# Kernel optimization log

Hardware: AMD Instinct MI355X
Metric: run time of the kernel (lower is better)

## Reference

```python
import jax, jax.numpy as jnp
import numpy as np

N_NODES = 10000
N_EDGES = 320000
IN_DIM = 256
HID = 64
HEADS = 4
OUT_DIM = 64
NEG_SLOPE = 0.2


def setup_inputs() -> dict:
    key = jax.random.key(0)
    ks = jax.random.split(key, 10)
    s = 0.05
    return {
        "h": jax.random.normal(ks[0], (N_NODES, IN_DIM), jnp.float32),
        "src": jax.random.randint(ks[1], (N_EDGES,), 0, N_NODES, jnp.int32),
        "dst": jax.random.randint(ks[2], (N_EDGES,), 0, N_NODES, jnp.int32),
        "W1": jax.random.normal(ks[3], (IN_DIM, HEADS * HID), jnp.float32) * s,
        "al1": jax.random.normal(ks[4], (HEADS, HID), jnp.float32) * s,
        "ar1": jax.random.normal(ks[5], (HEADS, HID), jnp.float32) * s,
        "b1": jnp.zeros((HEADS * HID,), jnp.float32),
        "W2": jax.random.normal(ks[6], (HEADS * HID, OUT_DIM), jnp.float32) * s,
        "al2": jax.random.normal(ks[7], (1, OUT_DIM), jnp.float32) * s,
        "ar2": jax.random.normal(ks[8], (1, OUT_DIM), jnp.float32) * s,
        "b2": jnp.zeros((OUT_DIM,), jnp.float32),
    }


def _gatconv(h, W, al, ar, b, src, dst, n_heads, d_out):
    """DGL-style GATConv: project, edge-softmax attention, scatter-aggregate."""
    n = h.shape[0]
    feat = (h @ W).reshape(n, n_heads, d_out)          # [N,H,D]
    el = jnp.sum(feat * al, axis=-1)                   # [N,H]
    er = jnp.sum(feat * ar, axis=-1)                   # [N,H]
    e = jax.nn.leaky_relu(el[src] + er[dst], NEG_SLOPE)  # [E,H]
    # segment softmax over incoming edges of each dst node
    m = jax.ops.segment_max(e, dst, num_segments=n)    # [N,H]
    ex = jnp.exp(e - m[dst])                           # [E,H]
    denom = jax.ops.segment_sum(ex, dst, num_segments=n)  # [N,H]
    alpha = ex / denom[dst]                            # [E,H]
    msg = feat[src] * alpha[:, :, None]                # [E,H,D]
    out = jax.ops.segment_sum(msg, dst, num_segments=n)  # [N,H,D]
    return out + b.reshape(n_heads, d_out)


def reference(h, src, dst, W1, al1, ar1, b1, W2, al2, ar2, b2):
    h1 = _gatconv(h, W1, al1, ar1, b1, src, dst, HEADS, HID)
    h1 = jax.nn.elu(h1.reshape(N_NODES, HEADS * HID))  # flatten(1) then ELU
    h2 = _gatconv(h1, W2, al2, ar2, b2, src, dst, 1, OUT_DIM)
    return jnp.squeeze(h2, axis=1)  # [N, OUT_DIM]
```

## Files before the change

kernel.cpp:

```cpp
#include <hip/hip_runtime.h>
#include <hip/hip_bf16.h>
#include <stdint.h>

#define NN 10000
#define NE 320000
#define NH 4
#define BCAP 128

#define GEMM1_MB 79
#define GEMM1_BLOCKS (GEMM1_MB * 4)
#define BUILD_BLOCKS 1250

typedef __attribute__((ext_vector_type(8))) short s16x8;
typedef __attribute__((ext_vector_type(4))) float f32x4;
typedef __attribute__((ext_vector_type(8))) unsigned short u16x8;

static __device__ __forceinline__ float b2f(unsigned short u) {
    union { unsigned int i; float f; } x; x.i = ((unsigned int)u) << 16; return x.f;
}
static __device__ __forceinline__ unsigned short f2b(float f) {
    unsigned int u = __float_as_uint(f);
    unsigned int r = (u + 0x7fffu + ((u >> 16) & 1u)) >> 16;
    return (unsigned short)r;
}

__global__ __launch_bounds__(256) void k_prep(const unsigned short* __restrict__ hraw,
                        const void* __restrict__ W1, const void* __restrict__ W2,
                        const void* al1, const void* ar1, const void* b1,
                        const void* al2, const void* ar2, const void* b2,
                        unsigned short* __restrict__ W1T, unsigned short* __restrict__ W2T,
                        unsigned short* __restrict__ canon, int* __restrict__ cnt,
                        int* __restrict__ flag) {
    __shared__ int sb[256];
    int t = threadIdx.x;
    int c = 0;
    for (int i = t; i < 2048; i += 256) {
        unsigned short u = hraw[i];
        int e = (u >> 7) & 0xFF;
        c += (e >= 97 && e <= 157) ? 1 : 0;
    }
    sb[t] = c;
    __syncthreads();
    for (int o = 128; o > 0; o >>= 1) {
        if (t < o) sb[t] += sb[t + o];
        __syncthreads();
    }
    int isbf = (sb[0] >= 1741) ? 1 : 0;

    int idx = blockIdx.x * 256 + t;
    if (idx < 65536) {
        int n = idx >> 8, k = idx & 255;
        W1T[idx] = isbf ? ((const unsigned short*)W1)[k * 256 + n]
                        : f2b(((const float*)W1)[k * 256 + n]);
    } else if (idx < 81920) {
        int j = idx - 65536;
        int n = j >> 8, k = j & 255;
        W2T[j] = isbf ? ((const unsigned short*)W2)[k * 64 + n]
                      : f2b(((const float*)W2)[k * 64 + n]);
    } else if (idx < 82880) {
        int j = idx - 81920;
        const void* srcp; int q;
        if      (j < 256) { srcp = al1; q = j; }
        else if (j < 512) { srcp = ar1; q = j - 256; }
        else if (j < 768) { srcp = b1;  q = j - 512; }
        else if (j < 832) { srcp = al2; q = j - 768; }
        else if (j < 896) { srcp = ar2; q = j - 832; }
        else              { srcp = b2;  q = j - 896; }
        canon[j] = isbf ? ((const unsigned short*)srcp)[q] : f2b(((const float*)srcp)[q]);
    } else if (idx < 92880) {
        cnt[idx - 82880] = 0;
    } else if (idx == 92880) {
        flag[0] = isbf;
    }
}

#define BSTRIDE 264
static __device__ __forceinline__ void gemm_body(short* Bs,
                        const void* __restrict__ A, const unsigned short* __restrict__ BT,
                        unsigned short* __restrict__ C,
                        float* __restrict__ el, float* __restrict__ er,
                        const unsigned short* __restrict__ al,
                        const unsigned short* __restrict__ ar,
                        int M, int N, int H, int a_isbf, int mtile, int head) {
    int t = threadIdx.x;
    int wave = t >> 6, lane = t & 63;
    int m0 = mtile * 128;
    const unsigned short* Bh = BT + (size_t)head * 64 * 256;

#pragma unroll
    for (int i = 0; i < 8; ++i) {
        int idx = t + i * 256;
        int row = idx >> 5, chunk = idx & 31;
        *(s16x8*)&Bs[row * BSTRIDE + chunk * 8] =
            *(const s16x8*)&Bh[(size_t)row * 256 + chunk * 8];
    }
    __syncthreads();

    int kq = (lane >> 4) * 8;
    const unsigned short* Ab = (const unsigned short*)A;
    const float*          Af = (const float*)A;
    int aR[2];
#pragma unroll
    for (int mi = 0; mi < 2; ++mi) {
        int aRow = m0 + mi * 64 + wave * 16 + (lane & 15);
        aR[mi] = (aRow < M) ? aRow : M - 1;
    }
    f32x4 acc[2][4] = {};

#pragma unroll
    for (int k0 = 0; k0 < 256; k0 += 32) {
        s16x8 afr[2];
#pragma unroll
        for (int mi = 0; mi < 2; ++mi) {
            if (a_isbf) {
                afr[mi] = *(const s16x8*)&Ab[(size_t)aR[mi] * 256 + k0 + kq];
            } else {
                const float* pf = &Af[(size_t)aR[mi] * 256 + k0 + kq];
                float4 x0 = *(const float4*)pf;
                float4 x1 = *(const float4*)(pf + 4);
                afr[mi][0] = (short)f2b(x0.x); afr[mi][1] = (short)f2b(x0.y);
                afr[mi][2] = (short)f2b(x0.z); afr[mi][3] = (short)f2b(x0.w);
                afr[mi][4] = (short)f2b(x1.x); afr[mi][5] = (short)f2b(x1.y);
                afr[mi][6] = (short)f2b(x1.z); afr[mi][7] = (short)f2b(x1.w);
            }
        }
#pragma unroll
        for (int nt = 0; nt < 4; ++nt) {
            s16x8 bfr = *(const s16x8*)&Bs[(nt * 16 + (lane & 15)) * BSTRIDE + k0 + kq];
            acc[0][nt] = __builtin_amdgcn_mfma_f32_16x16x32_bf16(afr[0], bfr, acc[0][nt], 0, 0, 0);
            acc[1][nt] = __builtin_amdgcn_mfma_f32_16x16x32_bf16(afr[1], bfr, acc[1][nt], 0, 0, 0);
        }
    }

    float alv[4], arv[4];
#pragma unroll
    for (int nt = 0; nt < 4; ++nt) {
        int c = (lane & 15) + nt * 16;
        alv[nt] = b2f(al[head * 64 + c]);
        arv[nt] = b2f(ar[head * 64 + c]);
    }
    int col0 = head * 64 + (lane & 15);
#pragma unroll
    for (int mi = 0; mi < 2; ++mi) {
        int r0 = m0 + mi * 64 + wave * 16 + (lane >> 4) * 4;
        float cr[4][4];
#pragma unroll
        for (int nt = 0; nt < 4; ++nt) {
            int col = col0 + nt * 16;
#pragma unroll
            for (int i = 0; i < 4; ++i) {
                unsigned short cb = f2b(acc[mi][nt][i]);
                cr[nt][i] = b2f(cb);
                int r = r0 + i;
                if (r < M) C[(size_t)r * N + col] = cb;
            }
        }
#pragma unroll
        for (int i = 0; i < 4; ++i) {
            float pl = 0.f, pr = 0.f;
#pragma unroll
            for (int nt = 0; nt < 4; ++nt) {
                pl += cr[nt][i] * alv[nt];
                pr += cr[nt][i] * arv[nt];
            }
#pragma unroll
            for (int o = 1; o < 16; o <<= 1) {
                pl += __shfl_xor(pl, o, 64);
                pr += __shfl_xor(pr, o, 64);
            }
            int r = r0 + i;
            if ((lane & 15) == 0 && r < M) {
                el[(size_t)r * H + head] = pl;
                er[(size_t)r * H + head] = pr;
            }
        }
    }
}

__global__ __launch_bounds__(256) void k_g1b(const void* __restrict__ A,
                        const unsigned short* __restrict__ W1T,
                        unsigned short* __restrict__ feat1,
                        float* __restrict__ el, float* __restrict__ er,
                        const unsigned short* __restrict__ al,
                        const unsigned short* __restrict__ ar,
                        const int* __restrict__ flagp,
                        const int* __restrict__ src, const int* __restrict__ dst,
                        int* __restrict__ cnt, int* __restrict__ bucket) {
    __shared__ short Bs[64 * BSTRIDE];
    int bid = blockIdx.x;
    if (bid < GEMM1_BLOCKS) {
        int head = bid / GEMM1_MB;
        int mtile = bid - head * GEMM1_MB;
        gemm_body(Bs, A, W1T, feat1, el, er, al, ar, NN, 256, NH, flagp[0], mtile, head);
    } else {
        int i = (bid - GEMM1_BLOCKS) * 256 + threadIdx.x;
        if (i < NE) {
            int d = dst[i];
            int pos = atomicAdd(&cnt[d], 1);
            if (pos < BCAP) bucket[(d << 7) + pos] = src[i];
        }
    }
}

static __device__ __forceinline__ void edge1_unit(int node,
                        const int* __restrict__ cnt, const int* __restrict__ bucket,
                        const float* __restrict__ el, const float* __restrict__ er,
                        const unsigned short* __restrict__ feat,
                        const unsigned short* __restrict__ b1,
                        unsigned short* __restrict__ h1row, int lane) {
    int eg = lane >> 3, d8 = lane & 7;
    int end = cnt[node]; if (end > BCAP) end = BCAP;
    const int* bkt = bucket + ((size_t)node << 7);
    float4 er4 = *(const float4*)&er[(size_t)node * 4];

    if (end <= 64) {
        int s = 0;
        float w0 = 0.f, w1 = 0.f, w2 = 0.f, w3 = 0.f;
        if (lane < end) {
            s = bkt[lane];
            float4 el4 = *(const float4*)&el[(size_t)s * 4];
            float x0 = el4.x + er4.x; x0 = (x0 >= 0.f) ? x0 : 0.2f * x0;
            float x1 = el4.y + er4.y; x1 = (x1 >= 0.f) ? x1 : 0.2f * x1;
            float x2 = el4.z + er4.z; x2 = (x2 >= 0.f) ? x2 : 0.2f * x2;
            float x3 = el4.w + er4.w; x3 = (x3 >= 0.f) ? x3 : 0.2f * x3;
            w0 = __expf(x0); w1 = __expf(x1);
            w2 = __expf(x2); w3 = __expf(x3);
        }
        int niter = (end + 7) >> 3;
#pragma unroll
        for (int h = 0; h < 4; ++h) {
            float wh = (h == 0) ? w0 : (h == 1) ? w1 : (h == 2) ? w2 : w3;
            float a[8] = {};
            for (int i = 0; i < niter; ++i) {
                int idx = 8 * i + eg;
                float we = __shfl(wh, idx, 64);
                int   se = __shfl(s, idx, 64);
                u16x8 fv = *(const u16x8*)&feat[(((size_t)se * NH + h) << 6) + (d8 << 3)];
#pragma unroll
                for (int j = 0; j < 8; ++j) a[j] += we * b2f(fv[j]);
            }
            float ls = wh;
#pragma unroll
            for (int o = 1; o < 64; o <<= 1) ls += __shfl_xor(ls, o, 64);
#pragma unroll
            for (int j = 0; j < 8; ++j) {
                a[j] += __shfl_xor(a[j], 8, 64);
                a[j] += __shfl_xor(a[j], 16, 64);
                a[j] += __shfl_xor(a[j], 32, 64);
            }
            if (eg == 0) {
                float inv = (ls > 0.f) ? 1.f / ls : 0.f;
                u16x8 r;
#pragma unroll
                for (int j = 0; j < 8; ++j) {
                    float o = a[j] * inv + b2f(b1[h * 64 + d8 * 8 + j]);
                    o = (o > 0.f) ? o : (__expf(o) - 1.f);
                    r[j] = f2b(o);
                }
                *(u16x8*)&h1row[h * 64 + d8 * 8] = r;
            }
        }
    } else {
        float a[4][8] = {};
        float ls0 = 0.f, ls1 = 0.f, ls2 = 0.f, ls3 = 0.f;
        for (int base = 0; base < end; base += 64) {
            int c = base + lane;
            int s = 0;
            float w0 = 0.f, w1 = 0.f, w2 = 0.f, w3 = 0.f;
            if (c < end) {
                s = bkt[c];
                float4 el4 = *(const float4*)&el[(size_t)s * 4];
                float x0 = el4.x + er4.x; x0 = (x0 >= 0.f) ? x0 : 0.2f * x0;
                float x1 = el4.y + er4.y; x1 = (x1 >= 0.f) ? x1 : 0.2f * x1;
                float x2 = el4.z + er4.z; x2 = (x2 >= 0.f) ? x2 : 0.2f * x2;
                float x3 = el4.w + er4.w; x3 = (x3 >= 0.f) ? x3 : 0.2f * x3;
                w0 = __expf(x0); w1 = __expf(x1);
                w2 = __expf(x2); w3 = __expf(x3);
            }
            ls0 += w0; ls1 += w1; ls2 += w2; ls3 += w3;
            int cn = end - base; if (cn > 64) cn = 64;
            int niter = (cn + 7) >> 3;
#pragma unroll
            for (int h = 0; h < 4; ++h) {
                float wh = (h == 0) ? w0 : (h == 1) ? w1 : (h == 2) ? w2 : w3;
                for (int i = 0; i < niter; ++i) {
                    int idx = 8 * i + eg;
                    float we = __shfl(wh, idx, 64);
                    int   se = __shfl(s, idx, 64);
                    u16x8 fv = *(const u16x8*)&feat[(((size_t)se * NH + h) << 6) + (d8 << 3)];
#pragma unroll
                    for (int j = 0; j < 8; ++j) a[h][j] += we * b2f(fv[j]);
                }
            }
        }
#pragma unroll
        for (int h = 0; h < 4; ++h) {
            float ls = (h == 0) ? ls0 : (h == 1) ? ls1 : (h == 2) ? ls2 : ls3;
#pragma unroll
            for (int o = 1; o < 64; o <<= 1) ls += __shfl_xor(ls, o, 64);
#pragma unroll
            for (int j = 0; j < 8; ++j) {
                a[h][j] += __shfl_xor(a[h][j], 8, 64);
                a[h][j] += __shfl_xor(a[h][j], 16, 64);
                a[h][j] += __shfl_xor(a[h][j], 32, 64);
            }
            if (eg == 0) {
                float inv = (ls > 0.f) ? 1.f / ls : 0.f;
                u16x8 r;
#pragma unroll
                for (int j = 0; j < 8; ++j) {
                    float o = a[h][j] * inv + b2f(b1[h * 64 + d8 * 8 + j]);
                    o = (o > 0.f) ? o : (__expf(o) - 1.f);
                    r[j] = f2b(o);
                }
                *(u16x8*)&h1row[h * 64 + d8 * 8] = r;
            }
        }
    }
}

#define H1S 264
__global__ __launch_bounds__(512, 4) void k_e1g2(const int* __restrict__ cnt,
                        const int* __restrict__ bucket,
                        const float* __restrict__ el, const float* __restrict__ er,
                        const unsigned short* __restrict__ feat,
                        const unsigned short* __restrict__ b1,
                        const unsigned short* __restrict__ W2T,
                        const unsigned short* __restrict__ al2,
                        const unsigned short* __restrict__ ar2,
                        unsigned short* __restrict__ feat2,
                        float* __restrict__ el2, float* __restrict__ er2) {
    __shared__ unsigned short h1s[16 * H1S];
    __shared__ unsigned short f2s[16 * 72];
    int t = threadIdx.x;
    int wave = t >> 6, lane = t & 63;
    int nb0 = blockIdx.x * 16;

#pragma unroll
    for (int r = 0; r < 2; ++r) {
        int lrow = wave * 2 + r;
        edge1_unit(nb0 + lrow, cnt, bucket, el, er, feat, b1, &h1s[lrow * H1S], lane);
    }
    __syncthreads();

    if (wave < 4) {
        int m = lane & 15;
        int kq = (lane >> 4) * 8;
        int colB = wave * 16 + m;
        const unsigned short* wp = &W2T[(size_t)colB * 256];
        f32x4 acc = {};
#pragma unroll
        for (int k0 = 0; k0 < 256; k0 += 32) {
            s16x8 af = *(const s16x8*)&h1s[m * H1S + k0 + kq];
            s16x8 bf = *(const s16x8*)&wp[k0 + kq];
            acc = __builtin_amdgcn_mfma_f32_16x16x32_bf16(af, bf, acc, 0, 0, 0);
        }
        int r0 = (lane >> 4) * 4;
#pragma unroll
        for (int i = 0; i < 4; ++i) {
            unsigned short cb = f2b(acc[i]);
            int row = r0 + i;
            feat2[(size_t)(nb0 + row) * 64 + colB] = cb;
            f2s[row * 72 + colB] = cb;
        }
    }
    __syncthreads();

    if (wave == 0) {
        int c = lane & 15;
        float alv[4], arv[4];
#pragma unroll
        for (int nt = 0; nt < 4; ++nt) {
            alv[nt] = b2f(al2[c + nt * 16]);
            arv[nt] = b2f(ar2[c + nt * 16]);
        }
        int r0 = (lane >> 4) * 4;
#pragma unroll
        for (int i = 0; i < 4; ++i) {
            int row = r0 + i;
            float cr[4];
#pragma unroll
            for (int nt = 0; nt < 4; ++nt) cr[nt] = b2f(f2s[row * 72 + c + nt * 16]);
            float pl = 0.f, pr = 0.f;
#pragma unroll
            for (int nt = 0; nt < 4; ++nt) {
                pl += cr[nt] * alv[nt];
                pr += cr[nt] * arv[nt];
            }
#pragma unroll
            for (int o = 1; o < 16; o <<= 1) {
                pl += __shfl_xor(pl, o, 64);
                pr += __shfl_xor(pr, o, 64);
            }
            if ((lane & 15) == 0) {
                el2[nb0 + row] = pl;
                er2[nb0 + row] = pr;
            }
        }
    }
}

__global__ __launch_bounds__(256) void k_edge2(const int* __restrict__ cnt,
                        const int* __restrict__ bucket,
                        const float* __restrict__ el, const float* __restrict__ er,
                        const unsigned short* __restrict__ feat,
                        const unsigned short* __restrict__ b2,
                        void* __restrict__ out, const int* __restrict__ flagp) {
    int wave = threadIdx.x >> 6, lane = threadIdx.x & 63;
    int node = blockIdx.x * 4 + wave;
    if (node >= NN) return;
    int eg = lane >> 3, d8 = lane & 7;
    int isbf = flagp[0];
    int end = cnt[node]; if (end > BCAP) end = BCAP;
    const int* bkt = bucket + ((size_t)node << 7);
    float er_d = er[node];
    float lsum = 0.f;
    float a[8] = {};
    for (int base = 0; base < end; base += 64) {
        int c = base + lane;
        float wgt = 0.f; int s = 0;
        if (c < end) {
            s = bkt[c];
            float x = el[s] + er_d;
            x = (x >= 0.f) ? x : 0.2f * x;
            wgt = __expf(x);
        }
        lsum += wgt;
        int cn = end - base; if (cn > 64) cn = 64;
        int niter = (cn + 7) >> 3;
#pragma unroll 2
        for (int i = 0; i < niter; ++i) {
            int idx = 8 * i + eg;
            float we = __shfl(wgt, idx, 64);
            int   se = __shfl(s, idx, 64);
            u16x8 fv = *(const u16x8*)&feat[((size_t)se << 6) + (d8 << 3)];
#pragma unroll
            for (int j = 0; j < 8; ++j) a[j] += we * b2f(fv[j]);
        }
    }
#pragma unroll
    for (int o = 1; o < 64; o <<= 1) lsum += __shfl_xor(lsum, o, 64);
#pragma unroll
    for (int j = 0; j < 8; ++j) {
        a[j] += __shfl_xor(a[j], 8, 64);
        a[j] += __shfl_xor(a[j], 16, 64);
        a[j] += __shfl_xor(a[j], 32, 64);
    }
    if (eg == 0) {
        float inv = (lsum > 0.f) ? 1.f / lsum : 0.f;
        float o[8];
#pragma unroll
        for (int j = 0; j < 8; ++j) o[j] = a[j] * inv + b2f(b2[d8 * 8 + j]);
        size_t ob = ((size_t)node << 6) + d8 * 8;
        if (isbf) {
            u16x8 r;
#pragma unroll
            for (int j = 0; j < 8; ++j) r[j] = f2b(o[j]);
            *(u16x8*)&((unsigned short*)out)[ob] = r;
        } else {
            float4 r0, r1;
            r0.x = o[0]; r0.y = o[1]; r0.z = o[2]; r0.w = o[3];
            r1.x = o[4]; r1.y = o[5]; r1.z = o[6]; r1.w = o[7];
            *(float4*)&((float*)out)[ob] = r0;
            *(float4*)&((float*)out)[ob + 4] = r1;
        }
    }
}

extern "C" void kernel_launch(void* const* d_in, const int* in_sizes, int n_in,
                              void* d_out, int out_size, void* d_ws, size_t ws_size,
                              hipStream_t stream) {
    const void* h   = d_in[0];
    const int*  src = (const int*)d_in[1];
    const int*  dst = (const int*)d_in[2];
    const void* W1  = d_in[3];
    const void* al1 = d_in[4];
    const void* ar1 = d_in[5];
    const void* b1  = d_in[6];
    const void* W2  = d_in[7];
    const void* al2 = d_in[8];
    const void* ar2 = d_in[9];
    const void* b2  = d_in[10];

    char* w = (char*)d_ws;
    size_t off = 0;
    auto alloc = [&](size_t bytes) -> void* {
        void* p = w + off;
        off = (off + bytes + 255) & ~(size_t)255;
        return p;
    };
    int* flag               = (int*)alloc(8);
    int* cnt                = (int*)alloc(NN * 4);
    int* bucket             = (int*)alloc((size_t)NN * BCAP * 4);
    unsigned short* canon   = (unsigned short*)alloc(960 * 2);
    unsigned short* W1T     = (unsigned short*)alloc(256 * 256 * 2);
    unsigned short* W2T     = (unsigned short*)alloc(64 * 256 * 2);
    unsigned short* feat1   = (unsigned short*)alloc((size_t)NN * 256 * 2);
    float* el1              = (float*)alloc(NN * NH * 4);
    float* er1              = (float*)alloc(NN * NH * 4);
    unsigned short* feat2   = (unsigned short*)alloc((size_t)NN * 64 * 2);
    float* el2              = (float*)alloc(NN * 4);
    float* er2              = (float*)alloc(NN * 4);
    (void)ws_size; (void)in_sizes; (void)n_in; (void)out_size;

    unsigned short* cal1 = canon + 0;
    unsigned short* car1 = canon + 256;
    unsigned short* cb1  = canon + 512;
    unsigned short* cal2 = canon + 768;
    unsigned short* car2 = canon + 832;
    unsigned short* cb2  = canon + 896;

    k_prep<<<363, 256, 0, stream>>>((const unsigned short*)h, W1, W2,
                                    al1, ar1, b1, al2, ar2, b2,
                                    W1T, W2T, canon, cnt, flag);
    k_g1b<<<GEMM1_BLOCKS + BUILD_BLOCKS, 256, 0, stream>>>(h, W1T, feat1, el1, er1,
                                                           cal1, car1, flag,
                                                           src, dst, cnt, bucket);
    k_e1g2<<<NN / 16, 512, 0, stream>>>(cnt, bucket, el1, er1, feat1, cb1,
                                        W2T, cal2, car2, feat2, el2, er2);
    k_edge2<<<(NN + 3) / 4, 256, 0, stream>>>(cnt, bucket, el2, er2, feat2, cb2, d_out, flag);
}
```

Measured before the change: 159.1 us.

## Fuse head loop in edge aggregation, halve e1g2 block size, fast-path edge2

In the layer-1 edge aggregation for nodes with at most 64 edges, the four per-head passes are merged into one loop. It loads all four head slices of each source row per iteration, shuffles the source index only once, and accumulates four accumulators at the same time. The fused edge+GEMM2 kernel now uses 256-thread blocks covering 8 nodes instead of 512 threads covering 16, so all four waves run the MFMA and rows past 8 are masked off. The layer-2 edge kernel gets a single-chunk fast path with deeper unrolling. These changes aim for more memory-level parallelism and better load balance, at the cost of higher register pressure from 32 accumulators and half-wasted MFMA rows.

```diff
diff --git a/kernel.cpp b/kernel.cpp
--- a/kernel.cpp
+++ b/kernel.cpp
@@ -226,34 +226,54 @@
             w0 = __expf(x0); w1 = __expf(x1);
             w2 = __expf(x2); w3 = __expf(x3);
         }
+        float ls0 = w0, ls1 = w1, ls2 = w2, ls3 = w3;
+#pragma unroll
+        for (int o = 1; o < 64; o <<= 1) {
+            ls0 += __shfl_xor(ls0, o, 64);
+            ls1 += __shfl_xor(ls1, o, 64);
+            ls2 += __shfl_xor(ls2, o, 64);
+            ls3 += __shfl_xor(ls3, o, 64);
+        }
+        float a0[8] = {}, a1[8] = {}, a2[8] = {}, a3[8] = {};
         int niter = (end + 7) >> 3;
-#pragma unroll
-        for (int h = 0; h < 4; ++h) {
-            float wh = (h == 0) ? w0 : (h == 1) ? w1 : (h == 2) ? w2 : w3;
-            float a[8] = {};
-            for (int i = 0; i < niter; ++i) {
-                int idx = 8 * i + eg;
-                float we = __shfl(wh, idx, 64);
-                int   se = __shfl(s, idx, 64);
-                u16x8 fv = *(const u16x8*)&feat[(((size_t)se * NH + h) << 6) + (d8 << 3)];
-#pragma unroll
-                for (int j = 0; j < 8; ++j) a[j] += we * b2f(fv[j]);
-            }
-            float ls = wh;
-#pragma unroll
-            for (int o = 1; o < 64; o <<= 1) ls += __shfl_xor(ls, o, 64);
+#pragma unroll 2
+        for (int i = 0; i < niter; ++i) {
+            int idx = 8 * i + eg;
+            int   se  = __shfl(s, idx, 64);
+            float we0 = __shfl(w0, idx, 64);
+            float we1 = __shfl(w1, idx, 64);
+            float we2 = __shfl(w2, idx, 64);
+            float we3 = __shfl(w3, idx, 64);
+            const u16x8* fp = (const u16x8*)(feat + ((size_t)se << 8));
+            u16x8 f0 = fp[d8];
+            u16x8 f1 = fp[8 + d8];
+            u16x8 f2 = fp[16 + d8];
+            u16x8 f3 = fp[24 + d8];
 #pragma unroll
             for (int j = 0; j < 8; ++j) {
-                a[j] += __shfl_xor(a[j], 8, 64);
-                a[j] += __shfl_xor(a[j], 16, 64);
-                a[j] += __shfl_xor(a[j], 32, 64);
-            }
-            if (eg == 0) {
+                a0[j] += we0 * b2f(f0[j]);
+                a1[j] += we1 * b2f(f1[j]);
+                a2[j] += we2 * b2f(f2[j]);
+                a3[j] += we3 * b2f(f3[j]);
+            }
+        }
+#pragma unroll
+        for (int j = 0; j < 8; ++j) {
+            a0[j] += __shfl_xor(a0[j], 8, 64);  a0[j] += __shfl_xor(a0[j], 16, 64);  a0[j] += __shfl_xor(a0[j], 32, 64);
+            a1[j] += __shfl_xor(a1[j], 8, 64);  a1[j] += __shfl_xor(a1[j], 16, 64);  a1[j] += __shfl_xor(a1[j], 32, 64);
+            a2[j] += __shfl_xor(a2[j], 8, 64);  a2[j] += __shfl_xor(a2[j], 16, 64);  a2[j] += __shfl_xor(a2[j], 32, 64);
+            a3[j] += __shfl_xor(a3[j], 8, 64);  a3[j] += __shfl_xor(a3[j], 16, 64);  a3[j] += __shfl_xor(a3[j], 32, 64);
+        }
+        if (eg == 0) {
+#pragma unroll
+            for (int h = 0; h < 4; ++h) {
+                const float* ah = (h == 0) ? a0 : (h == 1) ? a1 : (h == 2) ? a2 : a3;
+                float ls = (h == 0) ? ls0 : (h == 1) ? ls1 : (h == 2) ? ls2 : ls3;
                 float inv = (ls > 0.f) ? 1.f / ls : 0.f;
                 u16x8 r;
 #pragma unroll
                 for (int j = 0; j < 8; ++j) {
-                    float o = a[j] * inv + b2f(b1[h * 64 + d8 * 8 + j]);
+                    float o = ah[j] * inv + b2f(b1[h * 64 + d8 * 8 + j]);
                     o = (o > 0.f) ? o : (__expf(o) - 1.f);
                     r[j] = f2b(o);
                 }
@@ -305,7 +325,8 @@
                 a[h][j] += __shfl_xor(a[h][j], 32, 64);
             }
             if (eg == 0) {
-                float inv = (ls > 0.f) ? 1.f / ls : 0.f;
+                float ls2v = ls;
+                float inv = (ls2v > 0.f) ? 1.f / ls2v : 0.f;
                 u16x8 r;
 #pragma unroll
                 for (int j = 0; j < 8; ++j) {
@@ -320,7 +341,7 @@
 }
 
 #define H1S 264
-__global__ __launch_bounds__(512, 4) void k_e1g2(const int* __restrict__ cnt,
+__global__ __launch_bounds__(256, 4) void k_e1g2(const int* __restrict__ cnt,
                         const int* __restrict__ bucket,
                         const float* __restrict__ el, const float* __restrict__ er,
                         const unsigned short* __restrict__ feat,
@@ -334,7 +355,7 @@
     __shared__ unsigned short f2s[16 * 72];
     int t = threadIdx.x;
     int wave = t >> 6, lane = t & 63;
-    int nb0 = blockIdx.x * 16;
+    int nb0 = blockIdx.x * 8;
 
 #pragma unroll
     for (int r = 0; r < 2; ++r) {
@@ -343,7 +364,7 @@
     }
     __syncthreads();
 
-    if (wave < 4) {
+    {
         int m = lane & 15;
         int kq = (lane >> 4) * 8;
         int colB = wave * 16 + m;
@@ -358,10 +379,12 @@
         int r0 = (lane >> 4) * 4;
 #pragma unroll
         for (int i = 0; i < 4; ++i) {
-            unsigned short cb = f2b(acc[i]);
             int row = r0 + i;
-            feat2[(size_t)(nb0 + row) * 64 + colB] = cb;
-            f2s[row * 72 + colB] = cb;
+            if (row < 8) {
+                unsigned short cb = f2b(acc[i]);
+                feat2[(size_t)(nb0 + row) * 64 + colB] = cb;
+                f2s[row * 72 + colB] = cb;
+            }
         }
     }
     __syncthreads();
@@ -380,7 +403,8 @@
             int row = r0 + i;
             float cr[4];
 #pragma unroll
-            for (int nt = 0; nt < 4; ++nt) cr[nt] = b2f(f2s[row * 72 + c + nt * 16]);
+            for (int nt = 0; nt < 4; ++nt)
+                cr[nt] = b2f(f2s[(row < 8 ? row : 0) * 72 + c + nt * 16]);
             float pl = 0.f, pr = 0.f;
 #pragma unroll
             for (int nt = 0; nt < 4; ++nt) {
@@ -392,7 +416,7 @@
                 pl += __shfl_xor(pl, o, 64);
                 pr += __shfl_xor(pr, o, 64);
             }
-            if ((lane & 15) == 0) {
+            if ((lane & 15) == 0 && row < 8) {
                 el2[nb0 + row] = pl;
                 er2[nb0 + row] = pr;
             }
@@ -400,7 +424,7 @@
     }
 }
 
-__global__ __launch_bounds__(256) void k_edge2(const int* __restrict__ cnt,
+__global__ __launch_bounds__(256, 4) void k_edge2(const int* __restrict__ cnt,
                         const int* __restrict__ bucket,
                         const float* __restrict__ el, const float* __restrict__ er,
                         const unsigned short* __restrict__ feat,
@@ -414,21 +438,20 @@
     int end = cnt[node]; if (end > BCAP) end = BCAP;
     const int* bkt = bucket + ((size_t)node << 7);
     float er_d = er[node];
-    float lsum = 0.f;
+    float lsum;
     float a[8] = {};
-    for (int base = 0; base < end; base += 64) {
-        int c = base + lane;
-        float wgt = 0.f; int s = 0;
-        if (c < end) {
-            s = bkt[c];
+
+    if (end <= 64) {
+        int s = 0; float wgt = 0.f;
+        if (lane < end) {
+            s = bkt[lane];
             float x = el[s] + er_d;
             x = (x >= 0.f) ? x : 0.2f * x;
             wgt = __expf(x);
         }
-        lsum += wgt;
-        int cn = end - base; if (cn > 64) cn = 64;
-        int niter = (cn + 7) >> 3;
-#pragma unroll 2
+        lsum = wgt;
+        int niter = (end + 7) >> 3;
+#pragma unroll 4
         for (int i = 0; i < niter; ++i) {
             int idx = 8 * i + eg;
             float we = __shfl(wgt, idx, 64);
@@ -436,6 +459,30 @@
             u16x8 fv = *(const u16x8*)&feat[((size_t)se << 6) + (d8 << 3)];
 #pragma unroll
             for (int j = 0; j < 8; ++j) a[j] += we * b2f(fv[j]);
+        }
+    } else {
+        lsum = 0.f;
+        for (int base = 0; base < end; base += 64) {
+            int c = base + lane;
+            float wgt = 0.f; int s = 0;
+            if (c < end) {
+                s = bkt[c];
+                float x = el[s] + er_d;
+                x = (x >= 0.f) ? x : 0.2f * x;
+                wgt = __expf(x);
+            }
+            lsum += wgt;
+            int cn = end - base; if (cn > 64) cn = 64;
+            int niter = (cn + 7) >> 3;
+#pragma unroll 2
+            for (int i = 0; i < niter; ++i) {
+                int idx = 8 * i + eg;
+                float we = __shfl(wgt, idx, 64);
+                int   se = __shfl(s, idx, 64);
+                u16x8 fv = *(const u16x8*)&feat[((size_t)se << 6) + (d8 << 3)];
+#pragma unroll
+                for (int j = 0; j < 8; ++j) a[j] += we * b2f(fv[j]);
+            }
         }
     }
 #pragma unroll
@@ -516,7 +563,7 @@
     k_g1b<<<GEMM1_BLOCKS + BUILD_BLOCKS, 256, 0, stream>>>(h, W1T, feat1, el1, er1,
                                                            cal1, car1, flag,
                                                            src, dst, cnt, bucket);
-    k_e1g2<<<NN / 16, 512, 0, stream>>>(cnt, bucket, el1, er1, feat1, cb1,
-                                        W2T, cal2, car2, feat2, el2, er2);
+    k_e1g2<<<NN / 8, 256, 0, stream>>>(cnt, bucket, el1, er1, feat1, cb1,
+                                       W2T, cal2, car2, feat2, el2, er2);
     k_edge2<<<(NN + 3) / 4, 256, 0, stream>>>(cnt, bucket, el2, er2, feat2, cb2, d_out, flag);
 }
```

New measurement: 156.0 us. -2.0%, faster.
